# Performance work log

Hardware: AMD Instinct MI355X
Metric: run time of the kernel (lower is better)

Reference implementation:

```python
import jax, jax.numpy as jnp
import numpy as np

N, E, FDIM, H = 50000, 1_600_000, 256, 128


def setup_inputs() -> dict:
    key = jax.random.key(0)
    ks = jax.random.split(key, 16)
    s = 0.05
    return {
        "node_features": jax.random.normal(ks[0], (N, FDIM), dtype=jnp.float32),
        "edge_index": jax.random.randint(ks[1], (2, E), 0, N, dtype=jnp.int64),
        # node encoder: Linear(F,H) -> ReLU -> Linear(H,H)
        "enc_w1": jax.random.normal(ks[2], (FDIM, H), dtype=jnp.float32) * s,
        "enc_b1": jnp.zeros((H,), dtype=jnp.float32),
        "enc_w2": jax.random.normal(ks[3], (H, H), dtype=jnp.float32) * s,
        "enc_b2": jnp.zeros((H,), dtype=jnp.float32),
        # three GCNConv layers (weight + bias each)
        "conv_w1": jax.random.normal(ks[4], (H, H), dtype=jnp.float32) * s,
        "conv_b1": jnp.zeros((H,), dtype=jnp.float32),
        "conv_w2": jax.random.normal(ks[5], (H, H), dtype=jnp.float32) * s,
        "conv_b2": jnp.zeros((H,), dtype=jnp.float32),
        "conv_w3": jax.random.normal(ks[6], (H, H), dtype=jnp.float32) * s,
        "conv_b3": jnp.zeros((H,), dtype=jnp.float32),
        # edge classifier: Linear(2H,H) -> ReLU -> Dropout(eval: identity) -> Linear(H,1) -> Sigmoid
        "cls_w1": jax.random.normal(ks[7], (2 * H, H), dtype=jnp.float32) * s,
        "cls_b1": jnp.zeros((H,), dtype=jnp.float32),
        "cls_w2": jax.random.normal(ks[8], (H, 1), dtype=jnp.float32) * s,
        "cls_b2": jnp.zeros((1,), dtype=jnp.float32),
    }


def _gcn_conv(x, w, b, src, dst, norm, n):
    # GCNConv: x' = scatter_add_dst(norm * (x W)[src]) + b  (self-loops already in src/dst/norm)
    xw = x @ w
    out = jax.ops.segment_sum(xw[src] * norm[:, None], dst, num_segments=n)
    return out + b


def reference(node_features, edge_index, enc_w1, enc_b1, enc_w2, enc_b2,
              conv_w1, conv_b1, conv_w2, conv_b2, conv_w3, conv_b3,
              cls_w1, cls_b1, cls_w2, cls_b2):
    n = node_features.shape[0]
    loops = jnp.arange(n, dtype=edge_index.dtype)
    src = jnp.concatenate([edge_index[0], loops])  # (E+N,)
    dst = jnp.concatenate([edge_index[1], loops])
    # symmetric normalization with self-loops (PyG gcn_norm defaults)
    deg = jax.ops.segment_sum(jnp.ones(src.shape, node_features.dtype), dst, num_segments=n)
    dis = jnp.where(deg > 0, jax.lax.rsqrt(jnp.maximum(deg, 1.0)), 0.0)
    norm = dis[src] * dis[dst]  # (E+N,)

    # node encoder
    x = jax.nn.relu(node_features @ enc_w1 + enc_b1) @ enc_w2 + enc_b2
    # stacked GCN layers
    x = jax.nn.relu(_gcn_conv(x, conv_w1, conv_b1, src, dst, norm, n))
    x = jax.nn.relu(_gcn_conv(x, conv_w2, conv_b2, src, dst, norm, n))
    x = _gcn_conv(x, conv_w3, conv_b3, src, dst, norm, n)

    # edge features: gather + concat  -> (E, 2H)
    ef = jnp.concatenate([x[edge_index[0]], x[edge_index[1]]], axis=1)
    h = jax.nn.relu(ef @ cls_w1 + cls_b1)  # Dropout is identity at eval
    scores = jax.nn.sigmoid(h @ cls_w2 + cls_b2)
    return scores.squeeze(-1)  # (E,)
```

## Files before the change

kernel.cpp:

```cpp
#include <hip/hip_runtime.h>
#include <math.h>

#define HDIM 128
#define BSH 7
#define MAXBUCK 512

typedef __attribute__((ext_vector_type(8))) short    bf16x8;
typedef __attribute__((ext_vector_type(4))) float    f32x4;
typedef __attribute__((ext_vector_type(2))) float    f32x2;
typedef __attribute__((ext_vector_type(8))) unsigned short u16x8;
typedef __attribute__((ext_vector_type(4))) unsigned short u16x4;
typedef __attribute__((ext_vector_type(2))) __fp16 f16x2;

__device__ __forceinline__ unsigned short f2bf(float f) {
    union { float f; unsigned int i; } c; c.f = f;
    unsigned int r = (c.i + 0x7fffu + ((c.i >> 16) & 1u)) >> 16;
    return (unsigned short)r;
}
__device__ __forceinline__ void f8x8_decp(uint2 v, f32x2* p) {
    p[0] = __builtin_amdgcn_cvt_pk_f32_fp8((int)v.x, false);
    p[1] = __builtin_amdgcn_cvt_pk_f32_fp8((int)v.x, true);
    p[2] = __builtin_amdgcn_cvt_pk_f32_fp8((int)v.y, false);
    p[3] = __builtin_amdgcn_cvt_pk_f32_fp8((int)v.y, true);
}
__device__ __forceinline__ void f8x16_dech(uint4 v, f16x2* h) {
    f32x2 p[8];
    p[0] = __builtin_amdgcn_cvt_pk_f32_fp8((int)v.x, false);
    p[1] = __builtin_amdgcn_cvt_pk_f32_fp8((int)v.x, true);
    p[2] = __builtin_amdgcn_cvt_pk_f32_fp8((int)v.y, false);
    p[3] = __builtin_amdgcn_cvt_pk_f32_fp8((int)v.y, true);
    p[4] = __builtin_amdgcn_cvt_pk_f32_fp8((int)v.z, false);
    p[5] = __builtin_amdgcn_cvt_pk_f32_fp8((int)v.z, true);
    p[6] = __builtin_amdgcn_cvt_pk_f32_fp8((int)v.w, false);
    p[7] = __builtin_amdgcn_cvt_pk_f32_fp8((int)v.w, true);
#pragma unroll
    for (int i = 0; i < 8; i++) h[i] = __builtin_amdgcn_cvt_pkrtz(p[i].x, p[i].y);
}
__device__ __forceinline__ f16x2 pkmax0(f16x2 a) {
    f16x2 r;
    asm("v_pk_max_f16 %0, %1, 0" : "=v"(r) : "v"(a));
    return r;
}
__device__ __forceinline__ float edot16(uint4 pv, const f16x2 (&qh)[8], const f16x2 (&wh)[8]) {
    f16x2 ph[8]; f8x16_dech(pv, ph);
    float acc = 0.f;
#pragma unroll
    for (int i = 0; i < 8; i++)
        acc = __builtin_amdgcn_fdot2(pkmax0(ph[i] + qh[i]), wh[i], acc, false);
    return acc;
}
__device__ __forceinline__ float fsigmoid(float x) {
    float e = __builtin_amdgcn_exp2f(-x * 1.44269504f);
    return __builtin_amdgcn_rcpf(1.f + e);
}

struct WEnt { const float* src; unsigned short* dst; int K; };
struct WAll { WEnt w[5]; };

__global__ __launch_bounds__(256) void k_prep_all(
    WAll all, const float* __restrict__ We2, const float* __restrict__ be2,
    const float* __restrict__ Wc1, unsigned short* __restrict__ WtF,
    float* __restrict__ bF, int* __restrict__ tot)
{
    int y = blockIdx.y;
    int i = blockIdx.x * 256 + threadIdx.x;
    if (y == 5) {
        if (i < 128 * HDIM) {
            int c = i >> 7, k = i & 127;
            float s = 0.f;
            for (int j = 0; j < 128; j++)
                s += We2[k * 128 + j] * Wc1[j * 128 + c];
            WtF[(size_t)c * 128 + k] = f2bf(s);
            if (i < 128) {
                float b = 0.f;
                for (int j = 0; j < 128; j++) b += be2[j] * Wc1[j * 128 + i];
                bF[i] = b;
            }
        }
        return;
    }
    WEnt e = all.w[y];
    int lim = e.K * HDIM;
    if (i >= lim) {
        if (y == 1) {
            int zi = i - lim;
            if (zi < MAXBUCK) tot[zi] = 0;
        }
        return;
    }
    int k = i >> 7, c = i & 127;
    e.dst[(size_t)c * e.K + k] = f2bf(e.src[i]);
}

__global__ __launch_bounds__(256) void k_hist(
    const int* __restrict__ dst, int* __restrict__ tot,
    int* __restrict__ hist, int E, int chunk, int nbuck)
{
    __shared__ int h[MAXBUCK];
    for (int i = threadIdx.x; i < MAXBUCK; i += 256) h[i] = 0;
    __syncthreads();
    int beg = blockIdx.x * chunk;
    int fin = min(beg + chunk, E);
    for (int e = beg + threadIdx.x; e < fin; e += 256)
        atomicAdd(&h[dst[e] >> BSH], 1);
    __syncthreads();
    for (int k = threadIdx.x; k < nbuck; k += 256) {
        int v = h[k];
        hist[(size_t)blockIdx.x * nbuck + k] = v;
        if (v) atomicAdd(&tot[k], v);
    }
}

__global__ __launch_bounds__(256) void k_scan_buckets(
    const int* __restrict__ tot, int* __restrict__ gcur, int* __restrict__ base, int nbuck,
    const float* __restrict__ w2src, unsigned short* __restrict__ w2h)
{
    __shared__ int a[MAXBUCK], b[MAXBUCK];
    int t = threadIdx.x;
    if (t < 128) w2h[t] = __builtin_bit_cast(unsigned short, (__fp16)w2src[t]);
    for (int i = t; i < MAXBUCK; i += 256) a[i] = (i < nbuck) ? tot[i] : 0;
    __syncthreads();
    int* s1 = a; int* s2 = b;
    for (int off = 1; off < MAXBUCK; off <<= 1) {
        for (int i = t; i < MAXBUCK; i += 256)
            s2[i] = s1[i] + ((i >= off) ? s1[i - off] : 0);
        __syncthreads();
        int* tmp = s1; s1 = s2; s2 = tmp;
    }
    for (int i = t; i < nbuck; i += 256) {
        int e = (i == 0) ? 0 : s1[i - 1];
        gcur[i] = e;
        base[i] = e;
    }
    if (t == 0) base[nbuck] = s1[nbuck - 1];
}

__global__ __launch_bounds__(256) void k_partition(
    const int* __restrict__ src, const int* __restrict__ dst,
    const int* __restrict__ hist, int* __restrict__ gcur,
    uint2* __restrict__ stag, int E, int chunk, int nbuck)
{
    __shared__ int h[MAXBUCK];
    int t = threadIdx.x;
    for (int k = t; k < nbuck; k += 256) {
        int v = hist[(size_t)blockIdx.x * nbuck + k];
        h[k] = v ? atomicAdd(&gcur[k], v) : 0;
    }
    __syncthreads();
    int beg = blockIdx.x * chunk;
    int fin = min(beg + chunk, E);
    for (int e = beg + t; e < fin; e += 256) {
        unsigned int d = (unsigned int)dst[e];
        unsigned int s = (unsigned int)src[e];
        int pos = atomicAdd(&h[d >> BSH], 1);
        stag[pos] = make_uint2(s | (d << 16), (unsigned int)e);
    }
}

__global__ __launch_bounds__(256) void k_bucket_csr(
    const int* __restrict__ base, const uint2* __restrict__ stag,
    int* __restrict__ row_ptr, int* __restrict__ col, uint2* __restrict__ epk,
    float* __restrict__ dis, int n, int nbuck)
{
    __shared__ int cl[128], sa[128], sb[128], cur[128];
    int k = blockIdx.x;
    int n0 = k << BSH;
    int t = threadIdx.x;
    if (t < 128) cl[t] = 0;
    __syncthreads();
    int b0 = base[k];
    int m = base[k + 1] - b0;
    const uint2* seg = stag + b0;
    for (int i = t; i < m; i += 256) atomicAdd(&cl[(seg[i].x >> 16) & 127], 1);
    __syncthreads();
    int cv = 0;
    if (t < 128) { cv = cl[t]; sa[t] = cv; }
    __syncthreads();
    int* s1 = sa; int* s2 = sb;
    for (int off = 1; off < 128; off <<= 1) {
        if (t < 128) s2[t] = s1[t] + ((t >= off) ? s1[t - off] : 0);
        __syncthreads();
        int* tmp = s1; s1 = s2; s2 = tmp;
    }
    if (t < 128) {
        int node = n0 + t;
        if (node < n) {
            int rpv = b0 + s1[t] - cv;
            row_ptr[node] = rpv;
            cur[t] = rpv;
            dis[node] = rsqrtf(1.0f + (float)cv);
        }
    }
    if (k == 0 && t == 0) row_ptr[n] = base[nbuck];
    __syncthreads();
    for (int i = t; i < m; i += 256) {
        uint2 e = seg[i];
        int pos = atomicAdd(&cur[(e.x >> 16) & 127], 1);
        int s = (int)(e.x & 0xffffu);
        col[pos] = s;
        epk[pos] = make_uint2((unsigned int)s, e.y);
    }
}

__global__ __launch_bounds__(256) void k_gemm_b(
    const unsigned short* __restrict__ X, const unsigned short* __restrict__ Wt,
    const float* __restrict__ bias, const float* __restrict__ scale,
    void* __restrict__ C, int M, int relu_out, int out_mode)
{
    __shared__ unsigned short sW[128 * 128];
    const int t = threadIdx.x;
#pragma unroll
    for (int i = 0; i < 8; i++) {
        int c = t + i * 256;
        int row = c >> 4, o = c & 15;
        int mt = row >> 4, r = row & 15, kc = o >> 2, q = o & 3;
        int lidx = (mt * 4 + kc) * 64 + q * 16 + r;
        *(uint4*)(sW + (size_t)lidx * 8) = *(const uint4*)(Wt + (size_t)c * 8);
    }
    __syncthreads();
    int wave = t >> 6, lane = t & 63;
    int quad = lane >> 4, r = lane & 15;
    int row0 = blockIdx.x * 64 + wave * 16;
    if (row0 >= M) return;
    const unsigned short* xp = X + (size_t)(row0 + r) * 128 + quad * 8;
    f32x4 acc[8];
#pragma unroll
    for (int mt = 0; mt < 8; mt++) acc[mt] = (f32x4){0.f, 0.f, 0.f, 0.f};
#pragma unroll
    for (int kc = 0; kc < 4; kc++) {
        bf16x8 xf = *(const bf16x8*)(xp + kc * 32);
#pragma unroll
        for (int mt = 0; mt < 8; mt++) {
            bf16x8 wf = *(const bf16x8*)(sW + ((size_t)((mt * 4 + kc) * 64 + lane)) * 8);
            acc[mt] = __builtin_amdgcn_mfma_f32_16x16x32_bf16(wf, xf, acc[mt], 0, 0, 0);
        }
    }
    float sc = scale ? scale[row0 + r] : 1.f;
    if (out_mode == 1) {
        unsigned char* cp = (unsigned char*)C + (size_t)(row0 + r) * HDIM + quad * 4;
#pragma unroll
        for (int mt = 0; mt < 8; mt++) {
            float v[4];
#pragma unroll
            for (int j = 0; j < 4; j++) {
                float x = acc[mt][j];
                if (bias) x += bias[mt * 16 + quad * 4 + j];
                if (relu_out) x = fmaxf(x, 0.f);
                v[j] = x * sc;
            }
            int wd = 0;
            wd = __builtin_amdgcn_cvt_pk_fp8_f32(v[0], v[1], wd, false);
            wd = __builtin_amdgcn_cvt_pk_fp8_f32(v[2], v[3], wd, true);
            *(unsigned int*)(cp + mt * 16) = (unsigned int)wd;
        }
    } else {
        unsigned short* cp = (unsigned short*)C + (size_t)(row0 + r) * HDIM + quad * 4;
#pragma unroll
        for (int mt = 0; mt < 8; mt++) {
            u16x4 o;
#pragma unroll
            for (int j = 0; j < 4; j++) {
                float v = acc[mt][j];
                if (bias) v += bias[mt * 16 + quad * 4 + j];
                if (relu_out) v = fmaxf(v, 0.f);
                o[j] = f2bf(v * sc);
            }
            *(u16x4*)(cp + mt * 16) = o;
        }
    }
}

__global__ __launch_bounds__(256) void k_gemm_pq(
    const unsigned short* __restrict__ X, const unsigned short* __restrict__ WtP,
    const unsigned short* __restrict__ WtQ, const float* __restrict__ biasP,
    unsigned char* __restrict__ P, unsigned char* __restrict__ Q, int M)
{
    __shared__ unsigned short sW[2 * 128 * 128];
    const int t = threadIdx.x;
#pragma unroll
    for (int i = 0; i < 8; i++) {
        int c = t + i * 256;
        int row = c >> 4, o = c & 15;
        int mt = row >> 4, r = row & 15, kc = o >> 2, q = o & 3;
        int lidx = (mt * 4 + kc) * 64 + q * 16 + r;
        *(uint4*)(sW + (size_t)lidx * 8)         = *(const uint4*)(WtP + (size_t)c * 8);
        *(uint4*)(sW + 16384 + (size_t)lidx * 8) = *(const uint4*)(WtQ + (size_t)c * 8);
    }
    __syncthreads();
    int wave = t >> 6, lane = t & 63;
    int quad = lane >> 4, r = lane & 15;
    int row0 = blockIdx.x * 64 + wave * 16;
    if (row0 >= M) return;
    const unsigned short* xp = X + (size_t)(row0 + r) * 128 + quad * 8;
    f32x4 accP[8], accQ[8];
#pragma unroll
    for (int mt = 0; mt < 8; mt++) {
        accP[mt] = (f32x4){0.f, 0.f, 0.f, 0.f};
        accQ[mt] = (f32x4){0.f, 0.f, 0.f, 0.f};
    }
#pragma unroll
    for (int kc = 0; kc < 4; kc++) {
        bf16x8 xf = *(const bf16x8*)(xp + kc * 32);
#pragma unroll
        for (int mt = 0; mt < 8; mt++) {
            bf16x8 wfp = *(const bf16x8*)(sW + ((size_t)((mt * 4 + kc) * 64 + lane)) * 8);
            bf16x8 wfq = *(const bf16x8*)(sW + 16384 + ((size_t)((mt * 4 + kc) * 64 + lane)) * 8);
            accP[mt] = __builtin_amdgcn_mfma_f32_16x16x32_bf16(wfp, xf, accP[mt], 0, 0, 0);
            accQ[mt] = __builtin_amdgcn_mfma_f32_16x16x32_bf16(wfq, xf, accQ[mt], 0, 0, 0);
        }
    }
    unsigned char* pp = P + (size_t)(row0 + r) * HDIM + quad * 4;
    unsigned char* qp = Q + (size_t)(row0 + r) * HDIM + quad * 4;
#pragma unroll
    for (int mt = 0; mt < 8; mt++) {
        int wdp = 0, wdq = 0;
        float p0 = accP[mt][0] + biasP[mt * 16 + quad * 4 + 0];
        float p1 = accP[mt][1] + biasP[mt * 16 + quad * 4 + 1];
        float p2 = accP[mt][2] + biasP[mt * 16 + quad * 4 + 2];
        float p3 = accP[mt][3] + biasP[mt * 16 + quad * 4 + 3];
        wdp = __builtin_amdgcn_cvt_pk_fp8_f32(p0, p1, wdp, false);
        wdp = __builtin_amdgcn_cvt_pk_fp8_f32(p2, p3, wdp, true);
        wdq = __builtin_amdgcn_cvt_pk_fp8_f32(accQ[mt][0], accQ[mt][1], wdq, false);
        wdq = __builtin_amdgcn_cvt_pk_fp8_f32(accQ[mt][2], accQ[mt][3], wdq, true);
        *(unsigned int*)(pp + mt * 16) = (unsigned int)wdp;
        *(unsigned int*)(qp + mt * 16) = (unsigned int)wdq;
    }
}

__global__ __launch_bounds__(256) void k_gemm_nf(
    const float* __restrict__ X, const unsigned short* __restrict__ Wt,
    const float* __restrict__ bias, unsigned short* __restrict__ C,
    int M, int relu_out)
{
    const int K = 256;
    __shared__ unsigned short sW[128 * 256];
    const int t = threadIdx.x;
#pragma unroll
    for (int i = 0; i < 16; i++) {
        int c = t + i * 256;
        int row = c >> 5, o = c & 31;
        int mt = row >> 4, r = row & 15, kc = o >> 2, q = o & 3;
        int lidx = (mt * 8 + kc) * 64 + q * 16 + r;
        *(uint4*)(sW + (size_t)lidx * 8) = *(const uint4*)(Wt + (size_t)c * 8);
    }
    __syncthreads();
    int wave = t >> 6, lane = t & 63;
    int quad = lane >> 4, r = lane & 15;
    int row0 = blockIdx.x * 64 + wave * 16;
    if (row0 >= M) return;
    const float* xp = X + (size_t)(row0 + r) * K + quad * 8;
    f32x4 acc[8];
#pragma unroll
    for (int mt = 0; mt < 8; mt++) acc[mt] = (f32x4){0.f, 0.f, 0.f, 0.f};
#pragma unroll 2
    for (int kc = 0; kc < 8; kc++) {
        float4 xa = *(const float4*)(xp + kc * 32);
        float4 xb = *(const float4*)(xp + kc * 32 + 4);
        bf16x8 xf;
        xf[0] = (short)f2bf(xa.x); xf[1] = (short)f2bf(xa.y);
        xf[2] = (short)f2bf(xa.z); xf[3] = (short)f2bf(xa.w);
        xf[4] = (short)f2bf(xb.x); xf[5] = (short)f2bf(xb.y);
        xf[6] = (short)f2bf(xb.z); xf[7] = (short)f2bf(xb.w);
#pragma unroll
        for (int mt = 0; mt < 8; mt++) {
            bf16x8 wf = *(const bf16x8*)(sW + ((size_t)((mt * 8 + kc) * 64 + lane)) * 8);
            acc[mt] = __builtin_amdgcn_mfma_f32_16x16x32_bf16(wf, xf, acc[mt], 0, 0, 0);
        }
    }
    unsigned short* cp = C + (size_t)(row0 + r) * HDIM + quad * 4;
#pragma unroll
    for (int mt = 0; mt < 8; mt++) {
        u16x4 o;
#pragma unroll
        for (int j = 0; j < 4; j++) {
            float v = acc[mt][j];
            if (bias) v += bias[mt * 16 + quad * 4 + j];
            if (relu_out) v = fmaxf(v, 0.f);
            o[j] = f2bf(v);
        }
        *(u16x4*)(cp + mt * 16) = o;
    }
}

__global__ __launch_bounds__(256) void k_aggregate_f8(
    const int* __restrict__ row_ptr, const int* __restrict__ col,
    const float* __restrict__ dis, const uint2* __restrict__ y8,
    const float* __restrict__ bias, unsigned short* __restrict__ out, int n, int relu_out)
{
    int wid = (blockIdx.x * 256 + threadIdx.x) >> 6;
    if (wid >= n) return;
    int lane = threadIdx.x & 63;
    int q = lane >> 4, t = lane & 15;
    f32x2 acc[4];
    {
        uint2 sv = y8[(size_t)wid * 16 + t];
        f32x2 p[4]; f8x8_decp(sv, p);
#pragma unroll
        for (int i = 0; i < 4; i++) acc[i] = (q == 0) ? p[i] : (f32x2){0.f, 0.f};
    }
    int beg = row_ptr[wid], end = row_ptr[wid + 1];
    int j = beg + q;
    for (; j + 28 < end; j += 32) {
        int s[8];
        uint2 v[8];
#pragma unroll
        for (int u = 0; u < 8; u++) s[u] = col[j + u * 4];
#pragma unroll
        for (int u = 0; u < 8; u++) v[u] = y8[(size_t)s[u] * 16 + t];
#pragma unroll
        for (int u = 0; u < 8; u++) {
            f32x2 p[4]; f8x8_decp(v[u], p);
#pragma unroll
            for (int i = 0; i < 4; i++) acc[i] += p[i];
        }
    }
    for (; j + 12 < end; j += 16) {
        int s0 = col[j], s1 = col[j + 4], s2 = col[j + 8], s3 = col[j + 12];
        uint2 v0 = y8[(size_t)s0 * 16 + t];
        uint2 v1 = y8[(size_t)s1 * 16 + t];
        uint2 v2 = y8[(size_t)s2 * 16 + t];
        uint2 v3 = y8[(size_t)s3 * 16 + t];
        f32x2 p0[4], p1[4], p2[4], p3[4];
        f8x8_decp(v0, p0); f8x8_decp(v1, p1); f8x8_decp(v2, p2); f8x8_decp(v3, p3);
#pragma unroll
        for (int i = 0; i < 4; i++) acc[i] += (p0[i] + p1[i]) + (p2[i] + p3[i]);
    }
    for (; j < end; j += 4) {
        int s = col[j];
        uint2 v = y8[(size_t)s * 16 + t];
        f32x2 p[4]; f8x8_decp(v, p);
#pragma unroll
        for (int i = 0; i < 4; i++) acc[i] += p[i];
    }
#pragma unroll
    for (int i = 0; i < 4; i++) {
        acc[i].x += __shfl_xor(acc[i].x, 16, 64);
        acc[i].y += __shfl_xor(acc[i].y, 16, 64);
        acc[i].x += __shfl_xor(acc[i].x, 32, 64);
        acc[i].y += __shfl_xor(acc[i].y, 32, 64);
    }
    if (q == 0) {
        float di = dis[wid];
        u16x8 o;
#pragma unroll
        for (int i = 0; i < 4; i++) {
            float v0 = di * acc[i].x + bias[t * 8 + i * 2];
            float v1 = di * acc[i].y + bias[t * 8 + i * 2 + 1];
            if (relu_out) { v0 = fmaxf(v0, 0.f); v1 = fmaxf(v1, 0.f); }
            o[i * 2]     = f2bf(v0);
            o[i * 2 + 1] = f2bf(v1);
        }
        *(u16x8*)(out + (size_t)wid * HDIM + t * 8) = o;
    }
}

__global__ __launch_bounds__(256) void k_edge_score_csr(
    const int* __restrict__ row_ptr, const uint2* __restrict__ epk,
    const uint4* __restrict__ P8, const uint4* __restrict__ Q8,
    const unsigned short* __restrict__ w2h, const float* __restrict__ b2,
    float* __restrict__ out, int n)
{
    int wid = (blockIdx.x * 256 + threadIdx.x) >> 6;
    if (wid >= n) return;
    int lane = threadIdx.x & 63;
    unsigned g = (unsigned)(lane >> 3), t = (unsigned)(lane & 7);
    f16x2 wh[8], qh[8];
    {
        uint4 wv0 = *(const uint4*)(w2h + t * 16);
        uint4 wv1 = *(const uint4*)(w2h + t * 16 + 8);
        wh[0] = __builtin_bit_cast(f16x2, wv0.x);
        wh[1] = __builtin_bit_cast(f16x2, wv0.y);
        wh[2] = __builtin_bit_cast(f16x2, wv0.z);
        wh[3] = __builtin_bit_cast(f16x2, wv0.w);
        wh[4] = __builtin_bit_cast(f16x2, wv1.x);
        wh[5] = __builtin_bit_cast(f16x2, wv1.y);
        wh[6] = __builtin_bit_cast(f16x2, wv1.z);
        wh[7] = __builtin_bit_cast(f16x2, wv1.w);
        uint4 qv = Q8[(unsigned)wid * 8u + t];
        f8x16_dech(qv, qh);
    }
    float bb = b2[0];
    int beg = row_ptr[wid], end = row_ptr[wid + 1];
    int j = beg + (int)g;
    for (; j + 8 < end; j += 16) {
        uint2 e0 = epk[j], e1 = epk[j + 8];
        uint4 p0 = P8[e0.x * 8u + t];
        uint4 p1 = P8[e1.x * 8u + t];
        float s0 = edot16(p0, qh, wh);
        float s1 = edot16(p1, qh, wh);
        s0 += __shfl_xor(s0, 4, 8); s1 += __shfl_xor(s1, 4, 8);
        s0 += __shfl_xor(s0, 2, 8); s1 += __shfl_xor(s1, 2, 8);
        s0 += __shfl_xor(s0, 1, 8); s1 += __shfl_xor(s1, 1, 8);
        float sv = (t == 0) ? s0 : s1;
        unsigned eid = (t == 0) ? e0.y : e1.y;
        if (t < 2)
            __builtin_nontemporal_store(fsigmoid(sv + bb), &out[eid]);
    }
    if (j < end) {
        uint2 e0 = epk[j];
        uint4 p0 = P8[e0.x * 8u + t];
        float s0 = edot16(p0, qh, wh);
        s0 += __shfl_xor(s0, 4, 8);
        s0 += __shfl_xor(s0, 2, 8);
        s0 += __shfl_xor(s0, 1, 8);
        if (t == 0)
            __builtin_nontemporal_store(fsigmoid(s0 + bb), &out[e0.y]);
    }
}

extern "C" void kernel_launch(void* const* d_in, const int* in_sizes, int n_in,
                              void* d_out, int out_size, void* d_ws, size_t ws_size,
                              hipStream_t stream) {
    const float* nf   = (const float*)d_in[0];
    const int*   ei   = (const int*)d_in[1];
    const float* ew1  = (const float*)d_in[2];
    const float* eb1  = (const float*)d_in[3];
    const float* ew2  = (const float*)d_in[4];
    const float* eb2  = (const float*)d_in[5];
    const float* cw1  = (const float*)d_in[6];
    const float* cb1  = (const float*)d_in[7];
    const float* cw2  = (const float*)d_in[8];
    const float* cb2  = (const float*)d_in[9];
    const float* cw3  = (const float*)d_in[10];
    const float* cb3  = (const float*)d_in[11];
    const float* clw1 = (const float*)d_in[12];
    const float* clb1 = (const float*)d_in[13];
    const float* clw2 = (const float*)d_in[14];
    const float* clb2 = (const float*)d_in[15];
    float* out = (float*)d_out;

    const int FD = 256;
    const int N = in_sizes[0] / FD;
    const int E = in_sizes[1] / 2;
    const int NBUCK = (N + 127) >> BSH;
    const int PBLK = 256;
    const int chunk = (E + PBLK - 1) / PBLK;

    size_t Np = ((size_t)N + 256) & ~(size_t)255;
    char* w = (char*)d_ws;
    float* dis     = (float*)w;            w += Np * 4;
    int*   tot     = (int*)w;              w += MAXBUCK * 4;
    int*   gcur    = (int*)w;              w += MAXBUCK * 4;
    int*   base    = (int*)w;              w += (MAXBUCK + 4) * 4;
    int*   hist    = (int*)w;              w += (size_t)PBLK * MAXBUCK * 4;
    int*   row_ptr = (int*)w;              w += Np * 4;
    uint2* stag    = (uint2*)w;            w += (size_t)E * 8;
    uint2* epk     = (uint2*)w;            w += (size_t)E * 8;
    int*   col     = (int*)w;              w += (((size_t)E * 4) + 255) & ~(size_t)255;
    unsigned short* bufA = (unsigned short*)w;  w += (size_t)N * HDIM * 2;
    unsigned short* bufB = (unsigned short*)w;  w += (size_t)N * HDIM * 2;
    unsigned short* bufC = (unsigned short*)w;  w += (size_t)N * HDIM * 2;
    unsigned char*  f8X  = (unsigned char*)w;   w += ((size_t)N * HDIM + 255) & ~(size_t)255;
    unsigned char*  f8P  = (unsigned char*)w;   w += ((size_t)N * HDIM + 255) & ~(size_t)255;
    unsigned char*  f8Q  = (unsigned char*)w;   w += ((size_t)N * HDIM + 255) & ~(size_t)255;
    unsigned short* wtE1 = (unsigned short*)w;  w += 256 * HDIM * 2;
    unsigned short* wtF  = (unsigned short*)w;  w += 128 * HDIM * 2;
    unsigned short* wtC2 = (unsigned short*)w;  w += 128 * HDIM * 2;
    unsigned short* wtC3 = (unsigned short*)w;  w += 128 * HDIM * 2;
    unsigned short* wtT  = (unsigned short*)w;  w += 128 * HDIM * 2;
    unsigned short* wtB  = (unsigned short*)w;  w += 128 * HDIM * 2;
    unsigned short* w2h  = (unsigned short*)w;  w += 256 * 2;
    float*          bF   = (float*)w;           w += 128 * 4;

    int gemm_grid = (N + 63) / 64;
    int ag = (N + 3) / 4;

    WAll wa;
    wa.w[0] = { ew1,               wtE1, 256 };
    wa.w[1] = { cw2,               wtC2, 128 };
    wa.w[2] = { cw3,               wtC3, 128 };
    wa.w[3] = { clw1,              wtT,  128 };
    wa.w[4] = { clw1 + 128 * HDIM, wtB,  128 };
    k_prep_all<<<dim3(128, 6), 256, 0, stream>>>(wa, ew2, eb2, cw1, wtF, bF, tot);

    k_hist<<<PBLK, 256, 0, stream>>>(ei + E, tot, hist, E, chunk, NBUCK);
    k_scan_buckets<<<1, 256, 0, stream>>>(tot, gcur, base, NBUCK, clw2, w2h);
    k_partition<<<PBLK, 256, 0, stream>>>(ei, ei + E, hist, gcur, stag, E, chunk, NBUCK);
    k_bucket_csr<<<NBUCK, 256, 0, stream>>>(base, stag, row_ptr, col, epk, dis, N, NBUCK);

    k_gemm_nf<<<gemm_grid, 256, 0, stream>>>(nf, wtE1, eb1, bufA, N, 1);

    k_gemm_b<<<gemm_grid, 256, 0, stream>>>(bufA, wtF, bF, dis, f8X, N, 0, 1);
    k_aggregate_f8<<<ag, 256, 0, stream>>>(row_ptr, col, dis, (const uint2*)f8X, cb1, bufC, N, 1);
    k_gemm_b<<<gemm_grid, 256, 0, stream>>>(bufC, wtC2, nullptr, dis, f8X, N, 0, 1);
    k_aggregate_f8<<<ag, 256, 0, stream>>>(row_ptr, col, dis, (const uint2*)f8X, cb2, bufA, N, 1);
    k_gemm_b<<<gemm_grid, 256, 0, stream>>>(bufA, wtC3, nullptr, dis, f8X, N, 0, 1);
    k_aggregate_f8<<<ag, 256, 0, stream>>>(row_ptr, col, dis, (const uint2*)f8X, cb3, bufB, N, 0);

    k_gemm_pq<<<gemm_grid, 256, 0, stream>>>(bufB, wtT, wtB, clb1, f8P, f8Q, N);

    k_edge_score_csr<<<ag, 256, 0, stream>>>(row_ptr, epk, (const uint4*)f8P, (const uint4*)f8Q,
                                             w2h, clb2, out, N);
}
```

Before: 439.0 us.

## Merge independent graph-preprocessing and GEMM stages into shared launches

Per-node degree is now counted with global atomics in the histogram kernel, so dis can be computed before CSR construction. The bucket scan, dis computation and the node-encoder GEMM are merged into one launch, and edge partitioning shares a launch with the first conv GEMM. This removes two kernel launches and lets the independent CSR-build work overlap with dense GEMM work. The cost is extra global atomics on a per-node counter array and a new scratch buffer that must be zeroed.

```diff
diff --git a/kernel.cpp b/kernel.cpp
--- a/kernel.cpp
+++ b/kernel.cpp
@@ -60,7 +60,7 @@
 __global__ __launch_bounds__(256) void k_prep_all(
     WAll all, const float* __restrict__ We2, const float* __restrict__ be2,
     const float* __restrict__ Wc1, unsigned short* __restrict__ WtF,
-    float* __restrict__ bF, int* __restrict__ tot)
+    float* __restrict__ bF, int* __restrict__ tot, int* __restrict__ cnt, int np)
 {
     int y = blockIdx.y;
     int i = blockIdx.x * 256 + threadIdx.x;
@@ -76,15 +76,18 @@
                 for (int j = 0; j < 128; j++) b += be2[j] * Wc1[j * 128 + i];
                 bF[i] = b;
             }
+        } else {
+            int zi = i - 128 * HDIM;
+            if (zi < MAXBUCK) tot[zi] = 0;
         }
         return;
     }
     WEnt e = all.w[y];
     int lim = e.K * HDIM;
     if (i >= lim) {
-        if (y == 1) {
-            int zi = i - lim;
-            if (zi < MAXBUCK) tot[zi] = 0;
+        if (y >= 1) {
+            int zi = (y - 1) * 16384 + (i - 16384);
+            if (zi >= 0 && zi < np) cnt[zi] = 0;
         }
         return;
     }
@@ -93,7 +96,7 @@
 }
 
 __global__ __launch_bounds__(256) void k_hist(
-    const int* __restrict__ dst, int* __restrict__ tot,
+    const int* __restrict__ dst, int* __restrict__ tot, int* __restrict__ cnt,
     int* __restrict__ hist, int E, int chunk, int nbuck)
 {
     __shared__ int h[MAXBUCK];
@@ -101,8 +104,11 @@
     __syncthreads();
     int beg = blockIdx.x * chunk;
     int fin = min(beg + chunk, E);
-    for (int e = beg + threadIdx.x; e < fin; e += 256)
-        atomicAdd(&h[dst[e] >> BSH], 1);
+    for (int e = beg + threadIdx.x; e < fin; e += 256) {
+        int d = dst[e];
+        atomicAdd(&h[d >> BSH], 1);
+        atomicAdd(&cnt[d], 1);
+    }
     __syncthreads();
     for (int k = threadIdx.x; k < nbuck; k += 256) {
         int v = h[k];
@@ -111,56 +117,162 @@
     }
 }
 
-__global__ __launch_bounds__(256) void k_scan_buckets(
+__global__ __launch_bounds__(256) void k_mid(
     const int* __restrict__ tot, int* __restrict__ gcur, int* __restrict__ base, int nbuck,
-    const float* __restrict__ w2src, unsigned short* __restrict__ w2h)
-{
-    __shared__ int a[MAXBUCK], b[MAXBUCK];
-    int t = threadIdx.x;
-    if (t < 128) w2h[t] = __builtin_bit_cast(unsigned short, (__fp16)w2src[t]);
-    for (int i = t; i < MAXBUCK; i += 256) a[i] = (i < nbuck) ? tot[i] : 0;
-    __syncthreads();
-    int* s1 = a; int* s2 = b;
-    for (int off = 1; off < MAXBUCK; off <<= 1) {
-        for (int i = t; i < MAXBUCK; i += 256)
-            s2[i] = s1[i] + ((i >= off) ? s1[i - off] : 0);
+    const float* __restrict__ w2src, unsigned short* __restrict__ w2h,
+    const int* __restrict__ cnt, float* __restrict__ dis, int n, int ndis,
+    const float* __restrict__ X, const unsigned short* __restrict__ Wt,
+    const float* __restrict__ bias, unsigned short* __restrict__ C, int M)
+{
+    __shared__ unsigned short sW[128 * 256];
+    const int bx = blockIdx.x;
+    const int t = threadIdx.x;
+    if (bx == 0) {
+        int* a = (int*)sW; int* b = a + MAXBUCK;
+        if (t < 128) w2h[t] = __builtin_bit_cast(unsigned short, (__fp16)w2src[t]);
+        for (int i = t; i < MAXBUCK; i += 256) a[i] = (i < nbuck) ? tot[i] : 0;
         __syncthreads();
-        int* tmp = s1; s1 = s2; s2 = tmp;
-    }
-    for (int i = t; i < nbuck; i += 256) {
-        int e = (i == 0) ? 0 : s1[i - 1];
-        gcur[i] = e;
-        base[i] = e;
-    }
-    if (t == 0) base[nbuck] = s1[nbuck - 1];
-}
-
-__global__ __launch_bounds__(256) void k_partition(
-    const int* __restrict__ src, const int* __restrict__ dst,
+        int* s1 = a; int* s2 = b;
+        for (int off = 1; off < MAXBUCK; off <<= 1) {
+            for (int i = t; i < MAXBUCK; i += 256)
+                s2[i] = s1[i] + ((i >= off) ? s1[i - off] : 0);
+            __syncthreads();
+            int* tmp = s1; s1 = s2; s2 = tmp;
+        }
+        for (int i = t; i < nbuck; i += 256) {
+            int e = (i == 0) ? 0 : s1[i - 1];
+            gcur[i] = e;
+            base[i] = e;
+        }
+        if (t == 0) base[nbuck] = s1[nbuck - 1];
+        return;
+    }
+    if (bx <= ndis) {
+        int node = (bx - 1) * 256 + t;
+        if (node < n) dis[node] = rsqrtf(1.0f + (float)cnt[node]);
+        return;
+    }
+    const int K = 256;
+#pragma unroll
+    for (int i = 0; i < 16; i++) {
+        int c = t + i * 256;
+        int row = c >> 5, o = c & 31;
+        int mt = row >> 4, r = row & 15, kc = o >> 2, q = o & 3;
+        int lidx = (mt * 8 + kc) * 64 + q * 16 + r;
+        *(uint4*)(sW + (size_t)lidx * 8) = *(const uint4*)(Wt + (size_t)c * 8);
+    }
+    __syncthreads();
+    int wave = t >> 6, lane = t & 63;
+    int quad = lane >> 4, r = lane & 15;
+    int row0 = (bx - 1 - ndis) * 64 + wave * 16;
+    if (row0 >= M) return;
+    const float* xp = X + (size_t)(row0 + r) * K + quad * 8;
+    f32x4 acc[8];
+#pragma unroll
+    for (int mt = 0; mt < 8; mt++) acc[mt] = (f32x4){0.f, 0.f, 0.f, 0.f};
+#pragma unroll 2
+    for (int kc = 0; kc < 8; kc++) {
+        float4 xa = *(const float4*)(xp + kc * 32);
+        float4 xb = *(const float4*)(xp + kc * 32 + 4);
+        bf16x8 xf;
+        xf[0] = (short)f2bf(xa.x); xf[1] = (short)f2bf(xa.y);
+        xf[2] = (short)f2bf(xa.z); xf[3] = (short)f2bf(xa.w);
+        xf[4] = (short)f2bf(xb.x); xf[5] = (short)f2bf(xb.y);
+        xf[6] = (short)f2bf(xb.z); xf[7] = (short)f2bf(xb.w);
+#pragma unroll
+        for (int mt = 0; mt < 8; mt++) {
+            bf16x8 wf = *(const bf16x8*)(sW + ((size_t)((mt * 8 + kc) * 64 + lane)) * 8);
+            acc[mt] = __builtin_amdgcn_mfma_f32_16x16x32_bf16(wf, xf, acc[mt], 0, 0, 0);
+        }
+    }
+    unsigned short* cp = C + (size_t)(row0 + r) * HDIM + quad * 4;
+#pragma unroll
+    for (int mt = 0; mt < 8; mt++) {
+        u16x4 o;
+#pragma unroll
+        for (int j = 0; j < 4; j++) {
+            float v = acc[mt][j];
+            v += bias[mt * 16 + quad * 4 + j];
+            v = fmaxf(v, 0.f);
+            o[j] = f2bf(v);
+        }
+        *(u16x4*)(cp + mt * 16) = o;
+    }
+}
+
+__global__ __launch_bounds__(256) void k_part_conv1(
+    const int* __restrict__ src, const int* __restrict__ dstp,
     const int* __restrict__ hist, int* __restrict__ gcur,
-    uint2* __restrict__ stag, int E, int chunk, int nbuck)
-{
-    __shared__ int h[MAXBUCK];
-    int t = threadIdx.x;
-    for (int k = t; k < nbuck; k += 256) {
-        int v = hist[(size_t)blockIdx.x * nbuck + k];
-        h[k] = v ? atomicAdd(&gcur[k], v) : 0;
-    }
-    __syncthreads();
-    int beg = blockIdx.x * chunk;
-    int fin = min(beg + chunk, E);
-    for (int e = beg + t; e < fin; e += 256) {
-        unsigned int d = (unsigned int)dst[e];
-        unsigned int s = (unsigned int)src[e];
-        int pos = atomicAdd(&h[d >> BSH], 1);
-        stag[pos] = make_uint2(s | (d << 16), (unsigned int)e);
+    uint2* __restrict__ stag, int E, int chunk, int nbuck,
+    const unsigned short* __restrict__ X, const unsigned short* __restrict__ Wt,
+    const float* __restrict__ bias, const float* __restrict__ scale,
+    unsigned char* __restrict__ C, int M)
+{
+    __shared__ unsigned short sW[128 * 128];
+    const int bx = blockIdx.x;
+    const int t = threadIdx.x;
+    if (bx < 256) {
+        int* h = (int*)sW;
+        for (int k = t; k < nbuck; k += 256) {
+            int v = hist[(size_t)bx * nbuck + k];
+            h[k] = v ? atomicAdd(&gcur[k], v) : 0;
+        }
+        __syncthreads();
+        int beg = bx * chunk;
+        int fin = min(beg + chunk, E);
+        for (int e = beg + t; e < fin; e += 256) {
+            unsigned int d = (unsigned int)dstp[e];
+            unsigned int s = (unsigned int)src[e];
+            int pos = atomicAdd(&h[d >> BSH], 1);
+            stag[pos] = make_uint2(s | (d << 16), (unsigned int)e);
+        }
+        return;
+    }
+#pragma unroll
+    for (int i = 0; i < 8; i++) {
+        int c = t + i * 256;
+        int row = c >> 4, o = c & 15;
+        int mt = row >> 4, r = row & 15, kc = o >> 2, q = o & 3;
+        int lidx = (mt * 4 + kc) * 64 + q * 16 + r;
+        *(uint4*)(sW + (size_t)lidx * 8) = *(const uint4*)(Wt + (size_t)c * 8);
+    }
+    __syncthreads();
+    int wave = t >> 6, lane = t & 63;
+    int quad = lane >> 4, r = lane & 15;
+    int row0 = (bx - 256) * 64 + wave * 16;
+    if (row0 >= M) return;
+    const unsigned short* xp = X + (size_t)(row0 + r) * 128 + quad * 8;
+    f32x4 acc[8];
+#pragma unroll
+    for (int mt = 0; mt < 8; mt++) acc[mt] = (f32x4){0.f, 0.f, 0.f, 0.f};
+#pragma unroll
+    for (int kc = 0; kc < 4; kc++) {
+        bf16x8 xf = *(const bf16x8*)(xp + kc * 32);
+#pragma unroll
+        for (int mt = 0; mt < 8; mt++) {
+            bf16x8 wf = *(const bf16x8*)(sW + ((size_t)((mt * 4 + kc) * 64 + lane)) * 8);
+            acc[mt] = __builtin_amdgcn_mfma_f32_16x16x32_bf16(wf, xf, acc[mt], 0, 0, 0);
+        }
+    }
+    float sc = scale[row0 + r];
+    unsigned char* cp = C + (size_t)(row0 + r) * HDIM + quad * 4;
+#pragma unroll
+    for (int mt = 0; mt < 8; mt++) {
+        float v[4];
+#pragma unroll
+        for (int j = 0; j < 4; j++)
+            v[j] = (acc[mt][j] + bias[mt * 16 + quad * 4 + j]) * sc;
+        int wd = 0;
+        wd = __builtin_amdgcn_cvt_pk_fp8_f32(v[0], v[1], wd, false);
+        wd = __builtin_amdgcn_cvt_pk_fp8_f32(v[2], v[3], wd, true);
+        *(unsigned int*)(cp + mt * 16) = (unsigned int)wd;
     }
 }
 
 __global__ __launch_bounds__(256) void k_bucket_csr(
     const int* __restrict__ base, const uint2* __restrict__ stag,
     int* __restrict__ row_ptr, int* __restrict__ col, uint2* __restrict__ epk,
-    float* __restrict__ dis, int n, int nbuck)
+    int n, int nbuck)
 {
     __shared__ int cl[128], sa[128], sb[128], cur[128];
     int k = blockIdx.x;
@@ -188,7 +300,6 @@
             int rpv = b0 + s1[t] - cv;
             row_ptr[node] = rpv;
             cur[t] = rpv;
-            dis[node] = rsqrtf(1.0f + (float)cv);
         }
     }
     if (k == 0 && t == 0) row_ptr[n] = base[nbuck];
@@ -324,61 +435,6 @@
         wdq = __builtin_amdgcn_cvt_pk_fp8_f32(accQ[mt][2], accQ[mt][3], wdq, true);
         *(unsigned int*)(pp + mt * 16) = (unsigned int)wdp;
         *(unsigned int*)(qp + mt * 16) = (unsigned int)wdq;
-    }
-}
-
-__global__ __launch_bounds__(256) void k_gemm_nf(
-    const float* __restrict__ X, const unsigned short* __restrict__ Wt,
-    const float* __restrict__ bias, unsigned short* __restrict__ C,
-    int M, int relu_out)
-{
-    const int K = 256;
-    __shared__ unsigned short sW[128 * 256];
-    const int t = threadIdx.x;
-#pragma unroll
-    for (int i = 0; i < 16; i++) {
-        int c = t + i * 256;
-        int row = c >> 5, o = c & 31;
-        int mt = row >> 4, r = row & 15, kc = o >> 2, q = o & 3;
-        int lidx = (mt * 8 + kc) * 64 + q * 16 + r;
-        *(uint4*)(sW + (size_t)lidx * 8) = *(const uint4*)(Wt + (size_t)c * 8);
-    }
-    __syncthreads();
-    int wave = t >> 6, lane = t & 63;
-    int quad = lane >> 4, r = lane & 15;
-    int row0 = blockIdx.x * 64 + wave * 16;
-    if (row0 >= M) return;
-    const float* xp = X + (size_t)(row0 + r) * K + quad * 8;
-    f32x4 acc[8];
-#pragma unroll
-    for (int mt = 0; mt < 8; mt++) acc[mt] = (f32x4){0.f, 0.f, 0.f, 0.f};
-#pragma unroll 2
-    for (int kc = 0; kc < 8; kc++) {
-        float4 xa = *(const float4*)(xp + kc * 32);
-        float4 xb = *(const float4*)(xp + kc * 32 + 4);
-        bf16x8 xf;
-        xf[0] = (short)f2bf(xa.x); xf[1] = (short)f2bf(xa.y);
-        xf[2] = (short)f2bf(xa.z); xf[3] = (short)f2bf(xa.w);
-        xf[4] = (short)f2bf(xb.x); xf[5] = (short)f2bf(xb.y);
-        xf[6] = (short)f2bf(xb.z); xf[7] = (short)f2bf(xb.w);
-#pragma unroll
-        for (int mt = 0; mt < 8; mt++) {
-            bf16x8 wf = *(const bf16x8*)(sW + ((size_t)((mt * 8 + kc) * 64 + lane)) * 8);
-            acc[mt] = __builtin_amdgcn_mfma_f32_16x16x32_bf16(wf, xf, acc[mt], 0, 0, 0);
-        }
-    }
-    unsigned short* cp = C + (size_t)(row0 + r) * HDIM + quad * 4;
-#pragma unroll
-    for (int mt = 0; mt < 8; mt++) {
-        u16x4 o;
-#pragma unroll
-        for (int j = 0; j < 4; j++) {
-            float v = acc[mt][j];
-            if (bias) v += bias[mt * 16 + quad * 4 + j];
-            if (relu_out) v = fmaxf(v, 0.f);
-            o[j] = f2bf(v);
-        }
-        *(u16x4*)(cp + mt * 16) = o;
     }
 }
 
@@ -539,6 +595,7 @@
     size_t Np = ((size_t)N + 256) & ~(size_t)255;
     char* w = (char*)d_ws;
     float* dis     = (float*)w;            w += Np * 4;
+    int*   cnt     = (int*)w;              w += Np * 4;
     int*   tot     = (int*)w;              w += MAXBUCK * 4;
     int*   gcur    = (int*)w;              w += MAXBUCK * 4;
     int*   base    = (int*)w;              w += (MAXBUCK + 4) * 4;
@@ -564,6 +621,7 @@
 
     int gemm_grid = (N + 63) / 64;
     int ag = (N + 3) / 4;
+    int ndis = (N + 255) / 256;
 
     WAll wa;
     wa.w[0] = { ew1,               wtE1, 256 };
@@ -571,16 +629,20 @@
     wa.w[2] = { cw3,               wtC3, 128 };
     wa.w[3] = { clw1,              wtT,  128 };
     wa.w[4] = { clw1 + 128 * HDIM, wtB,  128 };
-    k_prep_all<<<dim3(128, 6), 256, 0, stream>>>(wa, ew2, eb2, cw1, wtF, bF, tot);
-
-    k_hist<<<PBLK, 256, 0, stream>>>(ei + E, tot, hist, E, chunk, NBUCK);
-    k_scan_buckets<<<1, 256, 0, stream>>>(tot, gcur, base, NBUCK, clw2, w2h);
-    k_partition<<<PBLK, 256, 0, stream>>>(ei, ei + E, hist, gcur, stag, E, chunk, NBUCK);
-    k_bucket_csr<<<NBUCK, 256, 0, stream>>>(base, stag, row_ptr, col, epk, dis, N, NBUCK);
-
-    k_gemm_nf<<<gemm_grid, 256, 0, stream>>>(nf, wtE1, eb1, bufA, N, 1);
-
-    k_gemm_b<<<gemm_grid, 256, 0, stream>>>(bufA, wtF, bF, dis, f8X, N, 0, 1);
+    k_prep_all<<<dim3(128, 6), 256, 0, stream>>>(wa, ew2, eb2, cw1, wtF, bF, tot, cnt, (int)Np);
+
+    k_hist<<<PBLK, 256, 0, stream>>>(ei + E, tot, cnt, hist, E, chunk, NBUCK);
+
+    k_mid<<<1 + ndis + gemm_grid, 256, 0, stream>>>(
+        tot, gcur, base, NBUCK, clw2, w2h, cnt, dis, N, ndis,
+        nf, wtE1, eb1, bufA, N);
+
+    k_part_conv1<<<256 + gemm_grid, 256, 0, stream>>>(
+        ei, ei + E, hist, gcur, stag, E, chunk, NBUCK,
+        bufA, wtF, bF, dis, f8X, N);
+
+    k_bucket_csr<<<NBUCK, 256, 0, stream>>>(base, stag, row_ptr, col, epk, N, NBUCK);
+
     k_aggregate_f8<<<ag, 256, 0, stream>>>(row_ptr, col, dis, (const uint2*)f8X, cb1, bufC, N, 1);
     k_gemm_b<<<gemm_grid, 256, 0, stream>>>(bufC, wtC2, nullptr, dis, f8X, N, 0, 1);
     k_aggregate_f8<<<ag, 256, 0, stream>>>(row_ptr, col, dis, (const uint2*)f8X, cb2, bufA, N, 1);
```

New measurement: 494.1 us. +12.5%, slower.
